# Performance work log

Hardware: AMD Instinct MI355X
Metric: run time of the kernel (lower is better)

Reference implementation:

```python
import jax, jax.numpy as jnp
import numpy as np

HEADS = 8
DIM_HEAD = 64
SCALE = DIM_HEAD ** -0.5  # q scaling
EPS = 1e-5  # channel LayerNorm eps (float32)


def setup_inputs() -> dict:
    key = jax.random.key(0)
    ks = jax.random.split(key, 4)
    B, C, H, W = 8, 256, 64, 64
    hd = HEADS * DIM_HEAD  # 512
    x = jax.random.normal(ks[0], (B, C, H, W), dtype=jnp.float32)
    w_qkv = jax.random.normal(ks[1], (3 * hd, C), dtype=jnp.float32) * 0.02  # 1x1 conv, no bias
    w_out = jax.random.normal(ks[2], (C, hd), dtype=jnp.float32) * 0.02     # 1x1 conv
    b_out = jax.random.normal(ks[3], (C,), dtype=jnp.float32) * 0.02
    g_ln = jnp.ones((C,), dtype=jnp.float32)  # LayerNorm gamma
    return {"x": x, "w_qkv": w_qkv, "w_out": w_out, "b_out": b_out, "g_ln": g_ln}


def reference(x, w_qkv, w_out, b_out, g_ln):
    B, C, H, W = x.shape
    n = H * W
    hd = HEADS * DIM_HEAD
    # 1x1 conv == per-pixel matmul: [B,C,H,W] x [3hd,C] -> [B,3hd,H,W]
    qkv = jnp.einsum('bchw,oc->bohw', x, w_qkv).reshape(B, 3, HEADS, DIM_HEAD, n)
    q, k, v = qkv[:, 0], qkv[:, 1], qkv[:, 2]  # each [B,h,d,n]
    q = jax.nn.softmax(q, axis=-2) * SCALE      # softmax over head-dim d
    k = jax.nn.softmax(k, axis=-1)              # softmax over spatial n
    v = v / n
    context = jnp.einsum('bhdn,bhen->bhde', k, v)   # [B,h,d,e]
    out = jnp.einsum('bhde,bhdn->bhen', context, q)  # [B,h,e,n]
    out = out.reshape(B, hd, H, W)
    # to_out: 1x1 conv + bias, then channel-wise LayerNorm (gamma only)
    y = jnp.einsum('bchw,oc->bohw', out, w_out) + b_out[None, :, None, None]
    mean = jnp.mean(y, axis=1, keepdims=True)
    var = jnp.var(y, axis=1, keepdims=True)  # unbiased=False
    return (y - mean) * jax.lax.rsqrt(var + EPS) * g_ln[None, :, None, None]
```

## Files before the change

### kernel.cpp

```cpp
#include <hip/hip_runtime.h>
#include <stdint.h>


#define NB    8
#define CCH   256
#define NSP   4096
#define O3    1536
#define NH    8
#define DH    64
#define CSTR  136

typedef unsigned short u16;
typedef unsigned int   u32;
typedef __bf16 bf16;
typedef bf16  bf16x8 __attribute__((ext_vector_type(8)));
typedef float f32x4  __attribute__((ext_vector_type(4)));
typedef u16   u16x8  __attribute__((ext_vector_type(8)));
typedef u16   u16x4  __attribute__((ext_vector_type(4)));

__device__ __forceinline__ float b2f(u16 h) {
  union { u32 u; float f; } x; x.u = ((u32)h) << 16; return x.f;
}
__device__ __forceinline__ u16 f2b(float f) {
  union { float f; u32 u; } x; x.f = f;
  u32 r = x.u + 0x7fffu + ((x.u >> 16) & 1u);
  return (u16)(r >> 16);
}
__device__ __forceinline__ int detect_bf(const void* g) {
  return ((const u32*)g)[0] != 0x3F800000u;
}
__device__ __forceinline__ void ldg2lds16(const u16* g, u16* l) {
  __builtin_amdgcn_global_load_lds((const __attribute__((address_space(1))) void*)g,
                                   (__attribute__((address_space(3))) void*)l,
                                   16, 0, 0);
}

#define TSTR 68
__global__ __launch_bounds__(256) void k_prep(const void* __restrict__ xv,
                                              const void* __restrict__ wv,
                                              u16* __restrict__ xT,
                                              u16* __restrict__ Wb,
                                              float* __restrict__ S,
                                              const void* __restrict__ g_lnv) {
  const int isbf = detect_bf(g_lnv);
  const int t = threadIdx.x;
  if (blockIdx.z == 8) {
    const int tid = blockIdx.y * 64 + blockIdx.x;
    if (tid < 192) {
      const int idx = tid * 256 + t;
      const int row = idx >> 5, cu = idx & 31;
      const int ks = cu >> 2, qd = cu & 3;
      int didx;
      if (row < 512) {
        const int h = row >> 6, i = (row >> 4) & 3, fr = row & 15;
        didx = ((h * 8 + ks) * 4 + i) * 64 + qd * 16 + fr;
      } else {
        int h, mrow;
        if (row < 1024) { h = (row - 512) >> 6;  mrow = row & 63; }
        else            { h = (row - 1024) >> 6; mrow = 64 + (row & 63); }
        const int mh = mrow >> 6, i = (mrow >> 4) & 3, fr = mrow & 15;
        didx = 16384 + (((h * 2 + mh) * 8 + ks) * 4 + i) * 64 + qd * 16 + fr;
      }
      if (isbf) {
        reinterpret_cast<uint4*>(Wb)[didx] = reinterpret_cast<const uint4*>(wv)[idx];
      } else {
        float4 a = reinterpret_cast<const float4*>(wv)[idx * 2];
        float4 b = reinterpret_cast<const float4*>(wv)[idx * 2 + 1];
        ushort4 o0, o1;
        o0.x = f2b(a.x); o0.y = f2b(a.y); o0.z = f2b(a.z); o0.w = f2b(a.w);
        o1.x = f2b(b.x); o1.y = f2b(b.y); o1.z = f2b(b.z); o1.w = f2b(b.w);
        reinterpret_cast<ushort4*>(Wb)[didx * 2]     = o0;
        reinterpret_cast<ushort4*>(Wb)[didx * 2 + 1] = o1;
      }
    } else if (tid < 200) {
      reinterpret_cast<float2*>(S)[(tid - 192) * 256 + t] = (float2){0.f, 0.f};
    }
    return;
  }
  const int b = blockIdx.z, cb = blockIdx.y * 64, nb = blockIdx.x * 64;
  __shared__ u16 tile[64 * TSTR];
  if (isbf) {
    const u16* xb = (const u16*)xv;
#pragma unroll
    for (int rr = 0; rr < 2; ++rr) {
      const int u = t + 256 * rr;
      const int c = u >> 3, ch = u & 7;
      u16x8 v = *reinterpret_cast<const u16x8*>(
          xb + ((size_t)(b * CCH + cb + c) * NSP + nb + ch * 8));
      u16* dst = tile + c * TSTR + ch * 8;
      *reinterpret_cast<u16x4*>(dst)     = (u16x4){v[0], v[1], v[2], v[3]};
      *reinterpret_cast<u16x4*>(dst + 4) = (u16x4){v[4], v[5], v[6], v[7]};
    }
  } else {
    const float* xb = (const float*)xv;
#pragma unroll
    for (int rr = 0; rr < 4; ++rr) {
      const int u = t + 256 * rr;
      const int c = u >> 4, c4 = u & 15;
      float4 f = *reinterpret_cast<const float4*>(
          xb + ((size_t)(b * CCH + cb + c) * NSP + nb + c4 * 4));
      u16x4 o; o[0] = f2b(f.x); o[1] = f2b(f.y); o[2] = f2b(f.z); o[3] = f2b(f.w);
      *reinterpret_cast<u16x4*>(tile + c * TSTR + c4 * 4) = o;
    }
  }
  __syncthreads();
#pragma unroll
  for (int rr = 0; rr < 2; ++rr) {
    const int u = t + 256 * rr;
    const int n = u >> 3, cc = u & 7;
    u16x8 o;
#pragma unroll
    for (int e = 0; e < 8; ++e) o[e] = tile[(cc * 8 + e) * TSTR + n];
    *reinterpret_cast<u16x8*>(
        xT + ((size_t)(b * NSP + nb + n) * CCH + cb + cc * 8)) = o;
  }
}

__global__ __launch_bounds__(256) void k_kv_mfma(const u16* __restrict__ Wb,
                                                 const u16* __restrict__ xT,
                                                 float* __restrict__ S,
                                                 float* __restrict__ ctxp) {
  __shared__ __align__(16) u16 gbuf[8192];
  __shared__ __align__(16) u16 epi[64 * CSTR * 2];
  u16* ekS = epi;
  u16* vS  = epi + 64 * CSTR;

  const int b = blockIdx.z, h = blockIdx.y, g = blockIdx.x;
  const int t = threadIdx.x, w = t >> 6, l = t & 63;
  const int wn = (w & 1) * 64;
  const int fr = l & 15, quad = l >> 4;

  const u16* B = xT + (size_t)b * NSP * CCH;
  const int s0 = w * 2, s1 = s0 + 1;
  const int ra0 = s0 * 16 + (l >> 2);
  const int ra1 = s1 * 16 + (l >> 2);
  const int kcs = ((l & 3) ^ ((l >> 3) & 3)) * 8;
  const int fsw = (quad ^ ((fr >> 1) & 3)) * 8;
  const u16* AkF = Wb + 131072 + (size_t)(h * 2 + (w >> 1)) * 16384 + (size_t)l * 8;

  f32x4 c2[4];
#pragma unroll
  for (int j = 0; j < 4; ++j) c2[j] = (f32x4){0.f, 0.f, 0.f, 0.f};
  float sacc = 0.f;

#define STAGE_B(SUB, KK, BUF)                                                   \
  {                                                                             \
    const int n0_ = g * 512 + (SUB) * 128;                                      \
    const int k0_ = (KK) * 32;                                                  \
    u16* Bs_ = gbuf + (BUF) * 4096;                                             \
    ldg2lds16(B + (size_t)(n0_ + ra0) * 256 + k0_ + kcs, Bs_ + s0 * 512);       \
    ldg2lds16(B + (size_t)(n0_ + ra1) * 256 + k0_ + kcs, Bs_ + s1 * 512);       \
  }

  STAGE_B(0, 0, 0);
  bf16x8 afc[4], afn[4];
#pragma unroll
  for (int i = 0; i < 4; ++i)
    afc[i] = *reinterpret_cast<const bf16x8*>(AkF + i * 512);

  for (int sub = 0; sub < 4; ++sub) {
    f32x4 acc[4][4];
#pragma unroll
    for (int i = 0; i < 4; ++i)
#pragma unroll
      for (int j = 0; j < 4; ++j) acc[i][j] = (f32x4){0.f, 0.f, 0.f, 0.f};

#pragma unroll
    for (int kk = 0; kk < 8; ++kk) {
      const bool last = (sub == 3 && kk == 7);
      const int nk = (kk < 7) ? kk + 1 : 0;
      if (!last) {
        const int ns = (kk < 7) ? sub : sub + 1;
        STAGE_B(ns, nk, (kk + 1) & 1);
        asm volatile("s_waitcnt vmcnt(2)" ::: "memory");
      } else {
        asm volatile("s_waitcnt vmcnt(0)" ::: "memory");
      }
      __builtin_amdgcn_s_barrier();
      if (!last) {
#pragma unroll
        for (int i = 0; i < 4; ++i)
          afn[i] = *reinterpret_cast<const bf16x8*>(AkF + (nk * 4 + i) * 512);
      }
      const u16* Bs = gbuf + (kk & 1) * 4096;
      bf16x8 bg[4];
#pragma unroll
      for (int j = 0; j < 4; ++j)
        bg[j] = *reinterpret_cast<const bf16x8*>(Bs + (wn + j * 16 + fr) * 32 + fsw);
#pragma unroll
      for (int i = 0; i < 4; ++i)
#pragma unroll
        for (int j = 0; j < 4; ++j)
          acc[i][j] = __builtin_amdgcn_mfma_f32_16x16x32_bf16(afc[i], bg[j], acc[i][j], 0, 0, 0);
      __builtin_amdgcn_s_barrier();
      if (!last) {
#pragma unroll
        for (int i = 0; i < 4; ++i) afc[i] = afn[i];
      }
    }

    {
      u16* dstT = (w < 2) ? ekS : vS;
#pragma unroll
      for (int i = 0; i < 4; ++i)
#pragma unroll
        for (int r = 0; r < 4; ++r) {
          const int row = i * 16 + quad * 4 + r;
#pragma unroll
          for (int j = 0; j < 4; ++j) {
            float v = acc[i][j][r];
            if (w < 2) v = __expf(v);
            dstT[row * CSTR + wn + j * 16 + fr] = f2b(v);
          }
        }
    }
    asm volatile("s_waitcnt lgkmcnt(0)" ::: "memory");
    __builtin_amdgcn_s_barrier();

    {
      const int d = t >> 2, seg = t & 3;
      float s = 0.f;
      const u16* src = ekS + d * CSTR + seg * 32;
#pragma unroll
      for (int m = 0; m < 32; ++m) s += b2f(src[m]);
      s += __shfl_xor(s, 1);
      s += __shfl_xor(s, 2);
      sacc += s;
    }

#pragma unroll
    for (int k0 = 0; k0 < 128; k0 += 32) {
      bf16x8 af = *reinterpret_cast<const bf16x8*>(ekS + (w * 16 + fr) * CSTR + k0 + quad * 8);
#pragma unroll
      for (int j = 0; j < 4; ++j) {
        bf16x8 bg = *reinterpret_cast<const bf16x8*>(vS + (j * 16 + fr) * CSTR + k0 + quad * 8);
        c2[j] = __builtin_amdgcn_mfma_f32_16x16x32_bf16(af, bg, c2[j], 0, 0, 0);
      }
    }
  }

  float* cb = ctxp + ((size_t)g * 64 + b * NH + h) * 4096;
#pragma unroll
  for (int j = 0; j < 4; ++j)
#pragma unroll
    for (int r = 0; r < 4; ++r)
      cb[(w * 16 + quad * 4 + r) * 64 + j * 16 + fr] = c2[j][r];
  if ((t & 3) == 0) atomicAdd(&S[b * 512 + h * 64 + (t >> 2)], sacc);
#undef STAGE_B
}

__global__ __launch_bounds__(256) void k_fold(const float* __restrict__ ctxp,
                                              const void* __restrict__ w_outv,
                                              const float* __restrict__ S,
                                              u16* __restrict__ Mb,
                                              const void* __restrict__ g_lnv) {
  const int isbf = detect_bf(g_lnv);
  const int h = blockIdx.x, b = blockIdx.y, ds = blockIdx.z * 16;
  const int t = threadIdx.x;
  __shared__ float ctxS[16][64];
  __shared__ float invS[16];
  if (t < 16) invS[t] = (1.0f / 4096.0f) / S[b * 512 + h * 64 + ds + t];
  const size_t bhoff = (size_t)(b * NH + h) * 4096 + (size_t)ds * 64;
#pragma unroll
  for (int i = 0; i < 4; ++i) {
    const int idx = t + 256 * i;
    float s = 0.f;
#pragma unroll
    for (int ch = 0; ch < 8; ++ch)
      s += ctxp[(size_t)ch * 64 * 4096 + bhoff + idx];
    ctxS[idx >> 6][idx & 63] = s;
  }
  float wrow[64];
  if (isbf) {
    const u16* wsrc = (const u16*)w_outv + (size_t)t * 512 + h * DH;
#pragma unroll
    for (int e4 = 0; e4 < 64; e4 += 4) {
      ushort4 u = *reinterpret_cast<const ushort4*>(wsrc + e4);
      wrow[e4 + 0] = b2f(u.x); wrow[e4 + 1] = b2f(u.y);
      wrow[e4 + 2] = b2f(u.z); wrow[e4 + 3] = b2f(u.w);
    }
  } else {
    const float* wsrc = (const float*)w_outv + (size_t)t * 512 + h * DH;
#pragma unroll
    for (int e4 = 0; e4 < 64; e4 += 4) {
      float4 f = *reinterpret_cast<const float4*>(wsrc + e4);
      wrow[e4 + 0] = f.x; wrow[e4 + 1] = f.y;
      wrow[e4 + 2] = f.z; wrow[e4 + 3] = f.w;
    }
  }
  __syncthreads();
  const int w_ = t >> 5, i_ = (t >> 4) & 1, fr_ = t & 15;
  const int f_ = i_ + 2 * (ds >> 5);
  const int qa = (ds & 31) >> 3;
  u16* dstF = Mb + ((((size_t)(b * 8 + w_) * 8 + h) * 4 + f_) * 64 + fr_) * 8;
  u16x8 o0, o1;
  for (int d = 0; d < 16; ++d) {
    float s = 0.f;
#pragma unroll
    for (int e = 0; e < 64; e += 4) {
      float4 c4 = *reinterpret_cast<const float4*>(&ctxS[d][e]);
      s += wrow[e] * c4.x + wrow[e + 1] * c4.y + wrow[e + 2] * c4.z + wrow[e + 3] * c4.w;
    }
    const u16 v = f2b(s * invS[d]);
    if (d < 8) o0[d] = v; else o1[d - 8] = v;
  }
  *reinterpret_cast<u16x8*>(dstF + (size_t)qa * 128)       = o0;
  *reinterpret_cast<u16x8*>(dstF + (size_t)(qa + 1) * 128) = o1;
}

__global__ __launch_bounds__(512, 4) void k_qmq_ln(const u16* __restrict__ Wb,
                                                   const u16* __restrict__ xT,
                                                   const u16* __restrict__ Mb,
                                                   const void* __restrict__ b_outv,
                                                   const void* __restrict__ g_lnv,
                                                   void* __restrict__ outv) {
  __shared__ __align__(16) u16 pool[64 * 512];
  __shared__ float redS[8][4][16];
  __shared__ float redQ[8][4][16];
  __shared__ float gS[256], bS[256];

  const int isbf = detect_bf(g_lnv);
  const int b  = blockIdx.y;
  const int n0 = blockIdx.x * 64;
  const int t  = threadIdx.x, w = t >> 6, l = t & 63;
  const int fr = l & 15, quad = l >> 4;

  if (t < 256) {
    gS[t] = isbf ? b2f(((const u16*)g_lnv)[t]) : ((const float*)g_lnv)[t];
    bS[t] = isbf ? b2f(((const u16*)b_outv)[t]) : ((const float*)b_outv)[t];
  }

  {
    const u16* Bg = xT + (size_t)b * NSP * CCH;
#pragma unroll
    for (int s = 0; s < 4; ++s) {
      const int p = w * 4 + s;
      const int r = 2 * p + (l >> 5);
      const int g16 = (l & 31) ^ (r & 7);
      ldg2lds16(Bg + (size_t)(n0 + r) * 256 + g16 * 8, pool + p * 512);
    }
    asm volatile("s_waitcnt vmcnt(0)" ::: "memory");
    __syncthreads();
  }

  f32x4 qa[4][4];
#pragma unroll
  for (int i = 0; i < 4; ++i)
#pragma unroll
    for (int j = 0; j < 4; ++j) qa[i][j] = (f32x4){0.f, 0.f, 0.f, 0.f};

  {
    const u16* AqF = Wb + (size_t)w * 16384 + (size_t)l * 8;
    bf16x8 afc[4], afn[4];
#pragma unroll
    for (int i = 0; i < 4; ++i)
      afc[i] = *reinterpret_cast<const bf16x8*>(AqF + i * 512);
#pragma unroll
    for (int ks = 0; ks < 8; ++ks) {
      if (ks < 7) {
#pragma unroll
        for (int i = 0; i < 4; ++i)
          afn[i] = *reinterpret_cast<const bf16x8*>(AqF + ((ks + 1) * 4 + i) * 512);
      }
      const int k0 = ks * 32;
      bf16x8 bg[4];
#pragma unroll
      for (int j = 0; j < 4; ++j) {
        const int row = j * 16 + fr;
        const int c16 = (k0 >> 3) + quad;
        bg[j] = *reinterpret_cast<const bf16x8*>(
            pool + row * 256 + ((c16 ^ (row & 7)) << 3));
      }
#pragma unroll
      for (int i = 0; i < 4; ++i)
#pragma unroll
        for (int j = 0; j < 4; ++j)
          qa[i][j] = __builtin_amdgcn_mfma_f32_16x16x32_bf16(afc[i], bg[j], qa[i][j], 0, 0, 0);
      if (ks < 7) {
#pragma unroll
        for (int i = 0; i < 4; ++i) afc[i] = afn[i];
      }
    }
  }
  __syncthreads();

  const u16* AmF = Mb + ((size_t)(b * 8 + w) * 16384) + (size_t)l * 8;
  bf16x8 amc[4], amn[4];
#pragma unroll
  for (int f = 0; f < 4; ++f)
    amc[f] = *reinterpret_cast<const bf16x8*>(AmF + f * 512);

#pragma unroll
  for (int j = 0; j < 4; ++j) {
    float s = 0.f;
#pragma unroll
    for (int i = 0; i < 4; ++i)
#pragma unroll
      for (int r = 0; r < 4; ++r) { qa[i][j][r] = __expf(qa[i][j][r]); s += qa[i][j][r]; }
    s += __shfl_xor(s, 16);
    s += __shfl_xor(s, 32);
    const float inv = 0.125f / s;
    const int n   = j * 16 + fr;
    const int swz = (n & 7) << 4;
#pragma unroll
    for (int i = 0; i < 4; ++i) {
      ushort4 o;
      o.x = f2b(qa[i][j][0] * inv); o.y = f2b(qa[i][j][1] * inv);
      o.z = f2b(qa[i][j][2] * inv); o.w = f2b(qa[i][j][3] * inv);
      const int hd2 = (w * 64 + i * 16 + quad * 4) * 2;
      *reinterpret_cast<ushort4*>(
          reinterpret_cast<char*>(pool) + ((n * 1024 + hd2) ^ swz)) = o;
    }
  }
  __syncthreads();

  f32x4 acc[2][4];
#pragma unroll
  for (int i = 0; i < 2; ++i)
#pragma unroll
    for (int j = 0; j < 4; ++j) acc[i][j] = (f32x4){0.f, 0.f, 0.f, 0.f};

  {
#pragma unroll
    for (int kt = 0; kt < 8; ++kt) {
      if (kt < 7) {
#pragma unroll
        for (int f = 0; f < 4; ++f)
          amn[f] = *reinterpret_cast<const bf16x8*>(AmF + ((kt + 1) * 4 + f) * 512);
      }
      const int k0 = kt * 64;
      bf16x8 bg0[4], bg1[4];
#pragma unroll
      for (int j = 0; j < 4; ++j) {
        const int n = j * 16 + fr;
        const int o0 = (n * 1024 + k0 * 2 + quad * 16) ^ ((n & 7) << 4);
        const int o1 = (n * 1024 + (k0 + 32) * 2 + quad * 16) ^ ((n & 7) << 4);
        bg0[j] = *reinterpret_cast<const bf16x8*>(reinterpret_cast<const char*>(pool) + o0);
        bg1[j] = *reinterpret_cast<const bf16x8*>(reinterpret_cast<const char*>(pool) + o1);
      }
#pragma unroll
      for (int i = 0; i < 2; ++i)
#pragma unroll
        for (int j = 0; j < 4; ++j)
          acc[i][j] = __builtin_amdgcn_mfma_f32_16x16x32_bf16(amc[i], bg0[j], acc[i][j], 0, 0, 0);
#pragma unroll
      for (int i = 0; i < 2; ++i)
#pragma unroll
        for (int j = 0; j < 4; ++j)
          acc[i][j] = __builtin_amdgcn_mfma_f32_16x16x32_bf16(amc[i + 2], bg1[j], acc[i][j], 0, 0, 0);
      if (kt < 7) {
#pragma unroll
        for (int f = 0; f < 4; ++f) amc[f] = amn[f];
      }
    }
  }

  float ps[4] = {}, pq[4] = {};
#pragma unroll
  for (int i = 0; i < 2; ++i)
#pragma unroll
    for (int r = 0; r < 4; ++r) {
      const int c = w * 32 + i * 16 + quad * 4 + r;
      const float bi = bS[c];
#pragma unroll
      for (int j = 0; j < 4; ++j) {
        acc[i][j][r] += bi;
        ps[j] += acc[i][j][r];
        pq[j] += acc[i][j][r] * acc[i][j][r];
      }
    }
#pragma unroll
  for (int j = 0; j < 4; ++j) {
    ps[j] += __shfl_xor(ps[j], 16); ps[j] += __shfl_xor(ps[j], 32);
    pq[j] += __shfl_xor(pq[j], 16); pq[j] += __shfl_xor(pq[j], 32);
  }
  if (quad == 0) {
#pragma unroll
    for (int j = 0; j < 4; ++j) { redS[w][j][fr] = ps[j]; redQ[w][j][fr] = pq[j]; }
  }
  __syncthreads();
  float mean[4], inv[4];
#pragma unroll
  for (int j = 0; j < 4; ++j) {
    float s = 0.f, q = 0.f;
#pragma unroll
    for (int g = 0; g < 8; ++g) { s += redS[g][j][fr]; q += redQ[g][j][fr]; }
    const float mn = s * (1.0f / 256.0f);
    const float vr = q * (1.0f / 256.0f) - mn * mn;
    mean[j] = mn;
    inv[j] = rsqrtf(vr + 1e-5f);
  }

#pragma unroll
  for (int i = 0; i < 2; ++i)
#pragma unroll
    for (int r = 0; r < 4; ++r) {
      const int c = w * 32 + i * 16 + quad * 4 + r;
      const float g = gS[c];
#pragma unroll
      for (int j = 0; j < 4; ++j) {
        const int col = n0 + j * 16 + fr;
        const float o = (acc[i][j][r] - mean[j]) * inv[j] * g;
        const size_t idx = ((size_t)b * CCH + c) * NSP + col;
        if (isbf) ((u16*)outv)[idx] = f2b(o);
        else      ((float*)outv)[idx] = o;
      }
    }
}

extern "C" void kernel_launch(void* const* d_in, const int* in_sizes, int n_in,
                              void* d_out, int out_size, void* d_ws, size_t ws_size,
                              hipStream_t stream) {
  (void)in_sizes; (void)n_in; (void)out_size; (void)ws_size;
  const void* x     = d_in[0];
  const void* w_qkv = d_in[1];
  const void* w_out = d_in[2];
  const void* b_out = d_in[3];
  const void* g_ln  = d_in[4];

  char* ws = (char*)d_ws;
  u16*   Wb   = (u16*)(ws + 256);
  float* S    = (float*)(ws + 851968);
  u16*   xT   = (u16*)(ws + 1048576);
  float* ctxp = (float*)(ws + 17825792);
  u16*   Mb   = (u16*)(ws + 26214400);

  k_prep    <<<dim3(64, 4, 9),  256, 0, stream>>>(x, w_qkv, xT, Wb, S, g_ln);
  k_kv_mfma <<<dim3(8, NH, NB), 256, 0, stream>>>(Wb, xT, S, ctxp);
  k_fold    <<<dim3(NH, NB, 4), 256, 0, stream>>>(ctxp, w_out, S, Mb, g_ln);
  k_qmq_ln  <<<dim3(64, NB),    512, 0, stream>>>(Wb, xT, Mb, b_out, g_ln, d_out);
}
```

Measured before the change: 161.0 us.

## Fuse fold kernel into kv kernel via last-block atomic counter

Removes the separate k_fold launch by having the last of the 8 spatial-chunk blocks per (batch, head) reduce the partial contexts and fold them with w_out into Mb. It uses a global atomic counter, zeroed in k_prep, together with threadfences. This saves one kernel launch and its gap, but the fold work is now done by only 64 blocks, each handling all 64 d rows, instead of 256 blocks. That serialises the fold tail inside the kv kernel.

```diff
diff --git a/kernel.cpp b/kernel.cpp
--- a/kernel.cpp
+++ b/kernel.cpp
@@ -5,7 +5,6 @@
 #define NB    8
 #define CCH   256
 #define NSP   4096
-#define O3    1536
 #define NH    8
 #define DH    64
 #define CSTR  136
@@ -41,6 +40,7 @@
                                               u16* __restrict__ xT,
                                               u16* __restrict__ Wb,
                                               float* __restrict__ S,
+                                              int* __restrict__ cnt,
                                               const void* __restrict__ g_lnv) {
   const int isbf = detect_bf(g_lnv);
   const int t = threadIdx.x;
@@ -74,6 +74,8 @@
       }
     } else if (tid < 200) {
       reinterpret_cast<float2*>(S)[(tid - 192) * 256 + t] = (float2){0.f, 0.f};
+    } else if (tid == 200) {
+      if (t < 64) cnt[t] = 0;
     }
     return;
   }
@@ -119,7 +121,11 @@
 __global__ __launch_bounds__(256) void k_kv_mfma(const u16* __restrict__ Wb,
                                                  const u16* __restrict__ xT,
                                                  float* __restrict__ S,
-                                                 float* __restrict__ ctxp) {
+                                                 float* __restrict__ ctxp,
+                                                 const void* __restrict__ w_outv,
+                                                 u16* __restrict__ Mb,
+                                                 int* __restrict__ cnt,
+                                                 const void* __restrict__ g_lnv) {
   __shared__ __align__(16) u16 gbuf[8192];
   __shared__ __align__(16) u16 epi[64 * CSTR * 2];
   u16* ekS = epi;
@@ -246,29 +252,27 @@
     for (int r = 0; r < 4; ++r)
       cb[(w * 16 + quad * 4 + r) * 64 + j * 16 + fr] = c2[j][r];
   if ((t & 3) == 0) atomicAdd(&S[b * 512 + h * 64 + (t >> 2)], sacc);
-#undef STAGE_B
-}
-
-__global__ __launch_bounds__(256) void k_fold(const float* __restrict__ ctxp,
-                                              const void* __restrict__ w_outv,
-                                              const float* __restrict__ S,
-                                              u16* __restrict__ Mb,
-                                              const void* __restrict__ g_lnv) {
+
+  __threadfence();
+  __shared__ int lastF;
+  if (t == 0) lastF = (atomicAdd(&cnt[b * NH + h], 1) == 7);
+  __syncthreads();
+  if (!lastF) return;
+  __threadfence();
+
   const int isbf = detect_bf(g_lnv);
-  const int h = blockIdx.x, b = blockIdx.y, ds = blockIdx.z * 16;
-  const int t = threadIdx.x;
-  __shared__ float ctxS[16][64];
-  __shared__ float invS[16];
-  if (t < 16) invS[t] = (1.0f / 4096.0f) / S[b * 512 + h * 64 + ds + t];
-  const size_t bhoff = (size_t)(b * NH + h) * 4096 + (size_t)ds * 64;
-#pragma unroll
-  for (int i = 0; i < 4; ++i) {
+  float* ctxS = (float*)epi;
+  float* invS = (float*)gbuf;
+  if (t < 64) invS[t] = (1.0f / 4096.0f) / S[b * 512 + h * 64 + t];
+  const size_t bhoff = (size_t)(b * NH + h) * 4096;
+#pragma unroll
+  for (int i = 0; i < 16; ++i) {
     const int idx = t + 256 * i;
     float s = 0.f;
 #pragma unroll
     for (int ch = 0; ch < 8; ++ch)
       s += ctxp[(size_t)ch * 64 * 4096 + bhoff + idx];
-    ctxS[idx >> 6][idx & 63] = s;
+    ctxS[idx] = s;
   }
   float wrow[64];
   if (isbf) {
@@ -290,22 +294,28 @@
   }
   __syncthreads();
   const int w_ = t >> 5, i_ = (t >> 4) & 1, fr_ = t & 15;
-  const int f_ = i_ + 2 * (ds >> 5);
-  const int qa = (ds & 31) >> 3;
-  u16* dstF = Mb + ((((size_t)(b * 8 + w_) * 8 + h) * 4 + f_) * 64 + fr_) * 8;
-  u16x8 o0, o1;
-  for (int d = 0; d < 16; ++d) {
-    float s = 0.f;
-#pragma unroll
-    for (int e = 0; e < 64; e += 4) {
-      float4 c4 = *reinterpret_cast<const float4*>(&ctxS[d][e]);
-      s += wrow[e] * c4.x + wrow[e + 1] * c4.y + wrow[e + 2] * c4.z + wrow[e + 3] * c4.w;
-    }
-    const u16 v = f2b(s * invS[d]);
-    if (d < 8) o0[d] = v; else o1[d - 8] = v;
-  }
-  *reinterpret_cast<u16x8*>(dstF + (size_t)qa * 128)       = o0;
-  *reinterpret_cast<u16x8*>(dstF + (size_t)(qa + 1) * 128) = o1;
+#pragma unroll
+  for (int dsl = 0; dsl < 4; ++dsl) {
+    const int ds = dsl * 16;
+    const int f_ = i_ + 2 * (ds >> 5);
+    const int qa = (ds & 31) >> 3;
+    u16* dstF = Mb + ((((size_t)(b * 8 + w_) * 8 + h) * 4 + f_) * 64 + fr_) * 8;
+    u16x8 o0, o1;
+    for (int d = 0; d < 16; ++d) {
+      const int dd = ds + d;
+      float s = 0.f;
+#pragma unroll
+      for (int e = 0; e < 64; e += 4) {
+        f32x4 c4 = *reinterpret_cast<const f32x4*>(&ctxS[dd * 64 + e]);
+        s += wrow[e] * c4[0] + wrow[e + 1] * c4[1] + wrow[e + 2] * c4[2] + wrow[e + 3] * c4[3];
+      }
+      const u16 v = f2b(s * invS[dd]);
+      if (d < 8) o0[d] = v; else o1[d - 8] = v;
+    }
+    *reinterpret_cast<u16x8*>(dstF + (size_t)qa * 128)       = o0;
+    *reinterpret_cast<u16x8*>(dstF + (size_t)(qa + 1) * 128) = o1;
+  }
+#undef STAGE_B
 }
 
 __global__ __launch_bounds__(512, 4) void k_qmq_ln(const u16* __restrict__ Wb,
@@ -521,12 +531,12 @@
   char* ws = (char*)d_ws;
   u16*   Wb   = (u16*)(ws + 256);
   float* S    = (float*)(ws + 851968);
+  int*   cnt  = (int*)(ws + 868352);
   u16*   xT   = (u16*)(ws + 1048576);
   float* ctxp = (float*)(ws + 17825792);
   u16*   Mb   = (u16*)(ws + 26214400);
 
-  k_prep    <<<dim3(64, 4, 9),  256, 0, stream>>>(x, w_qkv, xT, Wb, S, g_ln);
-  k_kv_mfma <<<dim3(8, NH, NB), 256, 0, stream>>>(Wb, xT, S, ctxp);
-  k_fold    <<<dim3(NH, NB, 4), 256, 0, stream>>>(ctxp, w_out, S, Mb, g_ln);
+  k_prep    <<<dim3(64, 4, 9),  256, 0, stream>>>(x, w_qkv, xT, Wb, S, cnt, g_ln);
+  k_kv_mfma <<<dim3(8, NH, NB), 256, 0, stream>>>(Wb, xT, S, ctxp, w_out, Mb, cnt, g_ln);
   k_qmq_ln  <<<dim3(64, NB),    512, 0, stream>>>(Wb, xT, Mb, b_out, g_ln, d_out);
 }
```

Result: slower. 266.3 us (+65.5%).
